# Kernel optimization log

Hardware: AMD Instinct MI355X
Metric: run time of the kernel (lower is better)

Reference implementation:

```python
import jax, jax.numpy as jnp
import numpy as np
import math

B, S, D, H = 2, 2048, 1024, 16
DK = D // H


def setup_inputs() -> dict:
    key = jax.random.key(0)
    ks = jax.random.split(key, 12)
    sc = 0.02
    inp = {
        "k": jax.random.normal(ks[0], (B, S, D), jnp.float32),
        "q": jax.random.normal(ks[1], (B, S, D), jnp.float32),
        "v": jax.random.normal(ks[2], (B, S, D), jnp.float32),
        "mask": 1,
        "w_k": jax.random.normal(ks[3], (D, D), jnp.float32) * sc,
        "b_k": jax.random.normal(ks[4], (D,), jnp.float32) * sc,
        "w_q": jax.random.normal(ks[5], (D, D), jnp.float32) * sc,
        "b_q": jax.random.normal(ks[6], (D,), jnp.float32) * sc,
        "w_v": jax.random.normal(ks[7], (D, D), jnp.float32) * sc,
        "b_v": jax.random.normal(ks[8], (D,), jnp.float32) * sc,
        "w_o": jax.random.normal(ks[9], (D, D), jnp.float32) * sc,
        "b_o": jax.random.normal(ks[10], (D,), jnp.float32) * sc,
    }
    return inp


def _mha(k, q, v, mask, w_k, b_k, w_q, b_q, w_v, b_v, w_o, b_o):
    # torch Linear: x @ W.T + b  (W is [out, in])
    key = k @ w_k.T + b_k
    query = q @ w_q.T + b_q
    value = v @ w_v.T + b_v
    # [B, S, D] -> [B, H, S, DK]
    key = key.reshape(B, S, H, DK).transpose(0, 2, 1, 3)
    query = query.reshape(B, S, H, DK).transpose(0, 2, 1, 3)
    value = value.reshape(B, S, H, DK).transpose(0, 2, 1, 3)
    # NOTE: original multiplies by sqrt(d_k) (not divides) -- faithful.
    scores = jnp.einsum("bhqd,bhkd->bhqk", query, key) * math.sqrt(DK)
    if mask:
        causal = jnp.triu(jnp.ones((S, S), dtype=bool), k=1)
        scores = jnp.where(causal, -jnp.inf, scores)
    # dropout p=0.0 is identity (original applies dropout to scores pre-softmax)
    attn = jax.nn.softmax(scores, axis=-1)
    out = jnp.einsum("bhqk,bhkd->bhqd", attn, value)
    out = out.transpose(0, 2, 1, 3).reshape(B, S, D)
    return out @ w_o.T + b_o


def reference(k, q, v, mask, w_k, b_k, w_q, b_q, w_v, b_v, w_o, b_o):
    return _mha(k, q, v, mask, w_k, b_k, w_q, b_q, w_v, b_v, w_o, b_o)
```

## Files before the change

kernel.cpp:

```cpp
#include <hip/hip_runtime.h>


typedef float f32x4 __attribute__((ext_vector_type(4)));
typedef float f32x16 __attribute__((ext_vector_type(16)));
typedef unsigned int u32x4 __attribute__((ext_vector_type(4)));
typedef _Float16 f16x8 __attribute__((ext_vector_type(8)));
typedef __fp16 fp16x2 __attribute__((ext_vector_type(2)));

#define DEV static __device__ __forceinline__

DEV unsigned short f2h(float x) {
  _Float16 h = (_Float16)x;
  union { _Float16 h; unsigned short u; } v; v.h = h;
  return v.u;
}

DEV unsigned pkrtz(float a, float b) {
  union { fp16x2 h; unsigned u; } v;
  v.h = __builtin_amdgcn_cvt_pkrtz(a, b);
  return v.u;
}

DEV float fexp2(float x) { return __builtin_amdgcn_exp2f(x); }

DEV void pswap(unsigned& a, unsigned& b) {
  auto r = __builtin_amdgcn_permlane32_swap(a, b, false, false);
  a = r[0]; b = r[1];
}

DEV void swap_pair(float v, float& x, float& y) {
  union { float f; unsigned u; } in; in.f = v;
  auto r = __builtin_amdgcn_permlane32_swap(in.u, in.u, false, false);
  union { unsigned u; float f; } ox, oy; ox.u = r[0]; oy.u = r[1];
  x = ox.f; y = oy.f;
}

DEV f16x8 mkfrag(unsigned a, unsigned b, unsigned c, unsigned d) {
  union { unsigned u[4]; f16x8 v; } z;
  z.u[0] = a; z.u[1] = b; z.u[2] = c; z.u[3] = d;
  return z.v;
}

DEV void mfma16(f32x4& d, u32x4 a, u32x4 b) {
  asm("v_mfma_f32_16x16x32_f16 %0, %1, %2, %0" : "+v"(d) : "v"(a), "v"(b));
}

DEV void gload16(const void* g, void* l) {
  __builtin_amdgcn_global_load_lds(
      (const __attribute__((address_space(1))) unsigned int*)g,
      (__attribute__((address_space(3))) unsigned int*)l, 16, 0, 0);
}

#define VMCNT0() asm volatile("s_waitcnt vmcnt(0)" ::: "memory")
#define NOPG(a,b,c,d)  asm volatile("s_nop 7\n\ts_nop 7" : "+v"(a), "+v"(b), "+v"(c), "+v"(d))

__global__ __launch_bounds__(256) void cvt_all(
    const float* __restrict__ k, const float* __restrict__ q, const float* __restrict__ v,
    const float* __restrict__ wk, const float* __restrict__ wq, const float* __restrict__ wv,
    const float* __restrict__ wo, unsigned short* __restrict__ dst) {
  const int i = (blockIdx.x * 256 + threadIdx.x) * 4;
  const float* src; int off;
  if (i < 4194304)       { src = k;  off = 0; }
  else if (i < 8388608)  { src = q;  off = 4194304; }
  else if (i < 12582912) { src = v;  off = 8388608; }
  else if (i < 13631488) { src = wk; off = 12582912; }
  else if (i < 14680064) { src = wq; off = 13631488; }
  else if (i < 15728640) { src = wv; off = 14680064; }
  else                   { src = wo; off = 15728640; }
  float4 val = *(const float4*)(src + (i - off));
  ushort4 o;
  o.x = f2h(val.x); o.y = f2h(val.y); o.z = f2h(val.z); o.w = f2h(val.w);
  *(ushort4*)(dst + i) = o;
}

DEV void gemm_body(const unsigned short* __restrict__ A, const unsigned short* __restrict__ W,
                   const float* __restrict__ bias, void* __restrict__ out, int mode,
                   float oscale) {
  __shared__ alignas(16) char lds_a[2][8192];
  __shared__ alignas(16) char lds_b[2][8192];
  const int t = threadIdx.x;
  const int l = t & 63, g = l >> 4, c = l & 15, w = t >> 6;
  const int wr = w >> 1, wc = w & 1;
  const int m0 = blockIdx.y << 7, n0 = blockIdx.x << 7;

  f32x4 acc[4][4] = {};

  const int i0 = t, i1 = t + 256;
  const int ar0 = i0 >> 2, as0 = (i0 & 3) ^ (ar0 & 3);
  const int ar1 = i1 >> 2, as1 = (i1 & 3) ^ (ar1 & 3);
  const unsigned short* ga0 = A + (long)(m0 + ar0) * 1024 + as0 * 8;
  const unsigned short* ga1 = A + (long)(m0 + ar1) * 1024 + as1 * 8;
  const unsigned short* gb0 = W + (long)(n0 + ar0) * 1024 + as0 * 8;
  const unsigned short* gb1 = W + (long)(n0 + ar1) * 1024 + as1 * 8;
  const int lo0 = i0 * 16, lo1 = i1 * 16;

  int aoff[4], boff[4];
#pragma unroll
  for (int i = 0; i < 4; i++) {
    const int ra = (wr << 6) + (i << 4) + c;
    aoff[i] = ra * 64 + ((g << 4) ^ ((ra & 3) << 4));
    const int rb = (wc << 6) + (i << 4) + c;
    boff[i] = rb * 64 + ((g << 4) ^ ((rb & 3) << 4));
  }

  gload16(ga0, lds_a[0] + lo0);
  gload16(ga1, lds_a[0] + lo1);
  gload16(gb0, lds_b[0] + lo0);
  gload16(gb1, lds_b[0] + lo1);

  for (int kt = 0; kt < 32; kt++) {
    const int cur = kt & 1;
    VMCNT0();
    __builtin_amdgcn_s_barrier();
    if (kt + 1 < 32) {
      gload16(ga0 + ((kt + 1) << 5), lds_a[cur ^ 1] + lo0);
      gload16(ga1 + ((kt + 1) << 5), lds_a[cur ^ 1] + lo1);
      gload16(gb0 + ((kt + 1) << 5), lds_b[cur ^ 1] + lo0);
      gload16(gb1 + ((kt + 1) << 5), lds_b[cur ^ 1] + lo1);
    }
    u32x4 af[4], bf[4];
#pragma unroll
    for (int i = 0; i < 4; i++) af[i] = *(const u32x4*)(lds_a[cur] + aoff[i]);
#pragma unroll
    for (int j = 0; j < 4; j++) bf[j] = *(const u32x4*)(lds_b[cur] + boff[j]);
#pragma unroll
    for (int i = 0; i < 4; i++)
#pragma unroll
      for (int j = 0; j < 4; j++)
        mfma16(acc[i][j], af[i], bf[j]);
  }

  NOPG(acc[0][0], acc[0][1], acc[0][2], acc[0][3]);
  NOPG(acc[1][0], acc[1][1], acc[1][2], acc[1][3]);
  NOPG(acc[2][0], acc[2][1], acc[2][2], acc[2][3]);
  NOPG(acc[3][0], acc[3][1], acc[3][2], acc[3][3]);

  if (mode == 1) {
#pragma unroll
    for (int j = 0; j < 4; j++) {
      const int n = n0 + (wc << 6) + (j << 4) + c;
      const float bb = bias[n];
      const int h = n >> 6, d = n & 63;
#pragma unroll
      for (int i = 0; i < 4; i++) {
        const int m = m0 + (wr << 6) + (i << 4) + (g << 2);
        const int b = m >> 11, s = m & 2047;
        ushort4 o;
        o.x = f2h(acc[i][j][0] + bb);
        o.y = f2h(acc[i][j][1] + bb);
        o.z = f2h(acc[i][j][2] + bb);
        o.w = f2h(acc[i][j][3] + bb);
        *(ushort4*)&((unsigned short*)out)[((long)((b << 4) + h) * 64 + d) * 2048 + s] = o;
      }
    }
  } else {
#pragma unroll
    for (int j = 0; j < 4; j++) {
      const int n = n0 + (wc << 6) + (j << 4) + c;
      const float bb = bias[n];
#pragma unroll
      for (int i = 0; i < 4; i++) {
#pragma unroll
        for (int r = 0; r < 4; r++) {
          const int m = m0 + (wr << 6) + (i << 4) + (g << 2) + r;
          const float val = (acc[i][j][r] + bb) * oscale;
          if (mode == 2) {
            ((float*)out)[(long)m * 1024 + n] = val;
          } else {
            const int b = m >> 11, s = m & 2047;
            const int h = n >> 6, d = n & 63;
            ((unsigned short*)out)[((long)((b << 4) + h) * 2048 + s) * 64 + d] = f2h(val);
          }
        }
      }
    }
  }
}

__global__ __launch_bounds__(256) void gemm_proj(
    const unsigned short* kb, const unsigned short* qb, const unsigned short* vb,
    const unsigned short* wkb, const unsigned short* wqb, const unsigned short* wvb,
    const float* bk, const float* bq, const float* bvv,
    unsigned short* Kp, unsigned short* Qp, unsigned short* VpT) {
  const int z = blockIdx.z;
  const unsigned short* A = (z == 0) ? kb : (z == 1) ? qb : vb;
  const unsigned short* W = (z == 0) ? wkb : (z == 1) ? wqb : wvb;
  const float* bias = (z == 0) ? bk : (z == 1) ? bq : bvv;
  void* out = (z == 0) ? (void*)Kp : (z == 1) ? (void*)Qp : (void*)VpT;
  const float sc = (z == 1) ? 11.5415603271f : 1.0f;
  gemm_body(A, W, bias, out, (z == 2) ? 1 : 0, sc);
}

__global__ __launch_bounds__(256) void gemm_out(
    const unsigned short* A, const unsigned short* W, const float* bias, float* out) {
  gemm_body(A, W, bias, out, 2, 1.0f);
}

__global__ __launch_bounds__(128) void attn_kernel(
    const unsigned short* __restrict__ Qp, const unsigned short* __restrict__ Kp,
    const unsigned short* __restrict__ VpT, unsigned short* __restrict__ O) {
  __shared__ alignas(16) char lds_k[2][8192];
  __shared__ alignas(16) char lds_v[2][8192];

  const int t = threadIdx.x;
  const int lane = t & 63, w = t >> 6;
  const int hi = lane >> 5, c32 = lane & 31;
  const int bh = blockIdx.x;
  const int qt = 31 - (int)blockIdx.y;
  const int qs = (qt << 6) + (w << 5);
  const int ntiles = qt + 1;

  const unsigned short* gk[4]; const unsigned short* gv[4]; int lofs[4];
#pragma unroll
  for (int n = 0; n < 4; n++) {
    const int idx = t + 128 * n;
    const int row = idx >> 3, sl = (idx & 7) ^ (row & 7);
    gk[n] = Kp + ((long)bh * 2048 + row) * 64 + sl * 8;
    gv[n] = VpT + ((long)bh * 64 + row) * 2048 + sl * 8;
    lofs[n] = idx * 16;
  }

  int koff[2][4];
#pragma unroll
  for (int x = 0; x < 2; x++)
#pragma unroll
    for (int y = 0; y < 4; y++) {
      const int row = 32 * x + c32;
      koff[x][y] = row * 128 + ((((y << 1) + hi) << 4) ^ ((row & 7) << 4));
    }

  const unsigned short* qrow = Qp + ((long)bh * 2048 + qs + c32) * 64 + hi * 8;
  f16x8 qf[4];
#pragma unroll
  for (int ks = 0; ks < 4; ks++) qf[ks] = *(const f16x8*)(qrow + ks * 16);

  f32x16 oT0 = {}, oT1 = {};
  float mrun = -1e30f, lrun = 0.f;
  const int qloc = (qs & 63) + c32;

#pragma unroll
  for (int n = 0; n < 4; n++) {
    gload16(gk[n], lds_k[0] + lofs[n]);
    gload16(gv[n], lds_v[0] + lofs[n]);
  }

  for (int tt = 0; tt < ntiles; tt++) {
    const int cur = tt & 1;
    VMCNT0();
    __builtin_amdgcn_s_barrier();
    if (tt + 1 < ntiles) {
      const long kvn = (long)(tt + 1) << 6;
#pragma unroll
      for (int n = 0; n < 4; n++) {
        gload16(gk[n] + kvn * 64, lds_k[cur ^ 1] + lofs[n]);
        gload16(gv[n] + kvn,      lds_v[cur ^ 1] + lofs[n]);
      }
    }

    f32x16 s0 = {}, s1 = {};
    __builtin_amdgcn_s_setprio(1);
#pragma unroll
    for (int ks = 0; ks < 4; ks++) {
      const f16x8 a0 = *(const f16x8*)(lds_k[cur] + koff[0][ks]);
      const f16x8 a1 = *(const f16x8*)(lds_k[cur] + koff[1][ks]);
      s0 = __builtin_amdgcn_mfma_f32_32x32x16_f16(a0, qf[ks], s0, 0, 0, 0);
      s1 = __builtin_amdgcn_mfma_f32_32x32x16_f16(a1, qf[ks], s1, 0, 0, 0);
    }
    __builtin_amdgcn_s_setprio(0);

    if (tt == qt) {
#pragma unroll
      for (int r = 0; r < 16; r++) {
        const int kvc = (r & 3) + 8 * (r >> 2) + 4 * hi;
        if (kvc > qloc)      s0[r] = -1e30f;
        if (kvc + 32 > qloc) s1[r] = -1e30f;
      }
    }

    float tm[16];
#pragma unroll
    for (int r = 0; r < 16; r++) tm[r] = fmaxf(s0[r], s1[r]);
#pragma unroll
    for (int d = 8; d >= 1; d >>= 1)
#pragma unroll
      for (int r = 0; r < 8; r++)
        if (r < d) tm[r] = fmaxf(tm[r], tm[r + d]);
    float x, y;
    swap_pair(tm[0], x, y);
    const float pmax = fmaxf(x, y);

    if (!__all(pmax - mrun <= 8.0f)) {
      const float mnew = fmaxf(mrun, pmax);
      const float corr = fexp2(mrun - mnew);
      mrun = mnew;
      lrun *= corr;
      oT0 *= corr;
      oT1 *= corr;
    }

#pragma unroll
    for (int r = 0; r < 16; r++) {
      s0[r] = fexp2(s0[r] - mrun);
      s1[r] = fexp2(s1[r] - mrun);
    }
    float ts[16];
#pragma unroll
    for (int r = 0; r < 16; r++) ts[r] = s0[r] + s1[r];
#pragma unroll
    for (int d = 8; d >= 1; d >>= 1)
#pragma unroll
      for (int r = 0; r < 8; r++)
        if (r < d) ts[r] = ts[r] + ts[r + d];
    lrun += ts[0];

    unsigned pk[8];
#pragma unroll
    for (int m = 0; m < 8; m++) pk[m] = pkrtz(s0[2 * m], s0[2 * m + 1]);
    pswap(pk[0], pk[2]); pswap(pk[1], pk[3]);
    pswap(pk[4], pk[6]); pswap(pk[5], pk[7]);
    const f16x8 pf0 = mkfrag(pk[0], pk[1], pk[2], pk[3]);
    const f16x8 pf1 = mkfrag(pk[4], pk[5], pk[6], pk[7]);
#pragma unroll
    for (int m = 0; m < 8; m++) pk[m] = pkrtz(s1[2 * m], s1[2 * m + 1]);
    pswap(pk[0], pk[2]); pswap(pk[1], pk[3]);
    pswap(pk[4], pk[6]); pswap(pk[5], pk[7]);
    const f16x8 pf2 = mkfrag(pk[0], pk[1], pk[2], pk[3]);
    const f16x8 pf3 = mkfrag(pk[4], pk[5], pk[6], pk[7]);

    __builtin_amdgcn_s_setprio(1);
    {
      const f16x8 v00 = *(const f16x8*)(lds_v[cur] + koff[0][0]);
      const f16x8 v01 = *(const f16x8*)(lds_v[cur] + koff[0][1]);
      const f16x8 v02 = *(const f16x8*)(lds_v[cur] + koff[0][2]);
      const f16x8 v03 = *(const f16x8*)(lds_v[cur] + koff[0][3]);
      oT0 = __builtin_amdgcn_mfma_f32_32x32x16_f16(v00, pf0, oT0, 0, 0, 0);
      oT0 = __builtin_amdgcn_mfma_f32_32x32x16_f16(v01, pf1, oT0, 0, 0, 0);
      oT0 = __builtin_amdgcn_mfma_f32_32x32x16_f16(v02, pf2, oT0, 0, 0, 0);
      oT0 = __builtin_amdgcn_mfma_f32_32x32x16_f16(v03, pf3, oT0, 0, 0, 0);
      const f16x8 v10 = *(const f16x8*)(lds_v[cur] + koff[1][0]);
      const f16x8 v11 = *(const f16x8*)(lds_v[cur] + koff[1][1]);
      const f16x8 v12 = *(const f16x8*)(lds_v[cur] + koff[1][2]);
      const f16x8 v13 = *(const f16x8*)(lds_v[cur] + koff[1][3]);
      oT1 = __builtin_amdgcn_mfma_f32_32x32x16_f16(v10, pf0, oT1, 0, 0, 0);
      oT1 = __builtin_amdgcn_mfma_f32_32x32x16_f16(v11, pf1, oT1, 0, 0, 0);
      oT1 = __builtin_amdgcn_mfma_f32_32x32x16_f16(v12, pf2, oT1, 0, 0, 0);
      oT1 = __builtin_amdgcn_mfma_f32_32x32x16_f16(v13, pf3, oT1, 0, 0, 0);
    }
    __builtin_amdgcn_s_setprio(0);
  }

  float sx, sy;
  swap_pair(lrun, sx, sy);
  const float inv = 1.0f / (sx + sy);
  const int b = bh >> 4, h = bh & 15;
  const long rowbase = ((long)b * 2048 + qs + c32) * 1024 + (h << 6);
#pragma unroll
  for (int dt = 0; dt < 2; dt++) {
#pragma unroll
    for (int g4 = 0; g4 < 4; g4++) {
      const f32x16& o = dt ? oT1 : oT0;
      uint2 pkd;
      pkd.x = pkrtz(o[4 * g4 + 0] * inv, o[4 * g4 + 1] * inv);
      pkd.y = pkrtz(o[4 * g4 + 2] * inv, o[4 * g4 + 3] * inv);
      *(uint2*)&O[rowbase + 32 * dt + 8 * g4 + 4 * hi] = pkd;
    }
  }
}

extern "C" void kernel_launch(void* const* d_in, const int* in_sizes, int n_in,
                              void* d_out, int out_size, void* d_ws, size_t ws_size,
                              hipStream_t stream) {
  (void)in_sizes; (void)n_in; (void)out_size; (void)ws_size;
  const float* kin = (const float*)d_in[0];
  const float* qin = (const float*)d_in[1];
  const float* vin = (const float*)d_in[2];
  const float* wk  = (const float*)d_in[4];
  const float* bk  = (const float*)d_in[5];
  const float* wq  = (const float*)d_in[6];
  const float* bq  = (const float*)d_in[7];
  const float* wv  = (const float*)d_in[8];
  const float* bv  = (const float*)d_in[9];
  const float* wo  = (const float*)d_in[10];
  const float* bo  = (const float*)d_in[11];

  unsigned short* ws  = (unsigned short*)d_ws;
  unsigned short* kb  = ws;
  unsigned short* qb  = ws + 4194304;
  unsigned short* vb  = ws + 8388608;
  unsigned short* wkb = ws + 12582912;
  unsigned short* wqb = ws + 13631488;
  unsigned short* wvb = ws + 14680064;
  unsigned short* wob = ws + 15728640;
  unsigned short* Kp  = ws + 16777216;
  unsigned short* Qp  = ws + 20971520;
  unsigned short* VpT = ws + 25165824;
  unsigned short* Oo  = ws + 29360128;

  cvt_all<<<16384, 256, 0, stream>>>(kin, qin, vin, wk, wq, wv, wo, ws);
  gemm_proj<<<dim3(8, 32, 3), 256, 0, stream>>>(kb, qb, vb, wkb, wqb, wvb,
                                                bk, bq, bv, Kp, Qp, VpT);
  attn_kernel<<<dim3(32, 32), 128, 0, stream>>>(Qp, Kp, VpT, Oo);
  gemm_out<<<dim3(8, 32), 256, 0, stream>>>(Oo, wob, bo, (float*)d_out);
}
```

Measured before the change: 130.5 us.

## Use single-wave attention blocks over 32-row query strips with 32-key tiles

The attention kernel changes from two-wave blocks covering 64 query rows with 64-key tiles to one-wave blocks covering 32 query rows with 32-key tiles. The grid doubles to 64 strips per head, and the V tile layout and swizzle are redone to fit the narrower tiles. The causal diagonal mask now covers only 32 keys, so less work is spent on masked-out entries, and the per-iteration block barrier is dropped. In exchange, K/V tiles are no longer shared between two waves, so global and LDS traffic per query row roughly doubles, and each iteration issues fewer MFMAs to amortize the softmax overhead.

```diff
diff --git a/kernel.cpp b/kernel.cpp
--- a/kernel.cpp
+++ b/kernel.cpp
@@ -1,11 +1,11 @@
 #include <hip/hip_runtime.h>
 
 
-typedef float f32x4 __attribute__((ext_vector_type(4)));
 typedef float f32x16 __attribute__((ext_vector_type(16)));
-typedef unsigned int u32x4 __attribute__((ext_vector_type(4)));
 typedef _Float16 f16x8 __attribute__((ext_vector_type(8)));
 typedef __fp16 fp16x2 __attribute__((ext_vector_type(2)));
+typedef float f32x4 __attribute__((ext_vector_type(4)));
+typedef unsigned int u32x4 __attribute__((ext_vector_type(4)));
 
 #define DEV static __device__ __forceinline__
 
@@ -196,37 +196,43 @@
   gemm_body(A, W, bias, out, 2, 1.0f);
 }
 
-__global__ __launch_bounds__(128) void attn_kernel(
+__global__ __launch_bounds__(64) void attn_kernel(
     const unsigned short* __restrict__ Qp, const unsigned short* __restrict__ Kp,
     const unsigned short* __restrict__ VpT, unsigned short* __restrict__ O) {
-  __shared__ alignas(16) char lds_k[2][8192];
-  __shared__ alignas(16) char lds_v[2][8192];
-
-  const int t = threadIdx.x;
-  const int lane = t & 63, w = t >> 6;
+  __shared__ alignas(16) char lds_k[2][4096];
+  __shared__ alignas(16) char lds_v[2][4096];
+
+  const int lane = threadIdx.x & 63;
   const int hi = lane >> 5, c32 = lane & 31;
   const int bh = blockIdx.x;
-  const int qt = 31 - (int)blockIdx.y;
-  const int qs = (qt << 6) + (w << 5);
-  const int ntiles = qt + 1;
-
-  const unsigned short* gk[4]; const unsigned short* gv[4]; int lofs[4];
+  const int strip = 63 - (int)blockIdx.y;
+  const int qs = strip << 5;
+  const int ntiles = strip + 1;
+
+  const unsigned short* gk[4]; const unsigned short* gv[4];
+  int lofsK[4], lofsV[4];
 #pragma unroll
   for (int n = 0; n < 4; n++) {
-    const int idx = t + 128 * n;
-    const int row = idx >> 3, sl = (idx & 7) ^ (row & 7);
-    gk[n] = Kp + ((long)bh * 2048 + row) * 64 + sl * 8;
-    gv[n] = VpT + ((long)bh * 64 + row) * 2048 + sl * 8;
-    lofs[n] = idx * 16;
-  }
-
-  int koff[2][4];
+    const int idx = lane + 64 * n;
+    const int rk = idx >> 3, sk = (idx & 7) ^ (rk & 7);
+    gk[n] = Kp + ((long)bh * 2048 + rk) * 64 + sk * 8;
+    lofsK[n] = idx * 16;
+    const int rv = idx >> 2, sv = (idx & 3) ^ ((rv >> 1) & 3);
+    gv[n] = VpT + ((long)bh * 64 + rv) * 2048 + sv * 8;
+    lofsV[n] = idx * 16;
+  }
+
+  int koffK[4];
+#pragma unroll
+  for (int ks = 0; ks < 4; ks++)
+    koffK[ks] = c32 * 128 + ((((ks << 1) + hi) ^ (c32 & 7)) << 4);
+  int koffV[2][2];
 #pragma unroll
   for (int x = 0; x < 2; x++)
 #pragma unroll
-    for (int y = 0; y < 4; y++) {
-      const int row = 32 * x + c32;
-      koff[x][y] = row * 128 + ((((y << 1) + hi) << 4) ^ ((row & 7) << 4));
+    for (int ks2 = 0; ks2 < 2; ks2++) {
+      const int row = (x << 5) + c32;
+      koffV[x][ks2] = row * 64 + (((((ks2 << 1) + hi)) ^ ((row >> 1) & 3)) << 4);
     }
 
   const unsigned short* qrow = Qp + ((long)bh * 2048 + qs + c32) * 64 + hi * 8;
@@ -236,54 +242,49 @@
 
   f32x16 oT0 = {}, oT1 = {};
   float mrun = -1e30f, lrun = 0.f;
-  const int qloc = (qs & 63) + c32;
 
 #pragma unroll
   for (int n = 0; n < 4; n++) {
-    gload16(gk[n], lds_k[0] + lofs[n]);
-    gload16(gv[n], lds_v[0] + lofs[n]);
+    gload16(gk[n], lds_k[0] + lofsK[n]);
+    gload16(gv[n], lds_v[0] + lofsV[n]);
   }
 
   for (int tt = 0; tt < ntiles; tt++) {
     const int cur = tt & 1;
     VMCNT0();
-    __builtin_amdgcn_s_barrier();
     if (tt + 1 < ntiles) {
-      const long kvn = (long)(tt + 1) << 6;
+      const long kvn = (long)(tt + 1) << 5;
 #pragma unroll
       for (int n = 0; n < 4; n++) {
-        gload16(gk[n] + kvn * 64, lds_k[cur ^ 1] + lofs[n]);
-        gload16(gv[n] + kvn,      lds_v[cur ^ 1] + lofs[n]);
+        gload16(gk[n] + kvn * 64, lds_k[cur ^ 1] + lofsK[n]);
+        gload16(gv[n] + kvn,      lds_v[cur ^ 1] + lofsV[n]);
       }
     }
 
-    f32x16 s0 = {}, s1 = {};
+    f32x16 s0 = {};
     __builtin_amdgcn_s_setprio(1);
 #pragma unroll
     for (int ks = 0; ks < 4; ks++) {
-      const f16x8 a0 = *(const f16x8*)(lds_k[cur] + koff[0][ks]);
-      const f16x8 a1 = *(const f16x8*)(lds_k[cur] + koff[1][ks]);
+      const f16x8 a0 = *(const f16x8*)(lds_k[cur] + koffK[ks]);
       s0 = __builtin_amdgcn_mfma_f32_32x32x16_f16(a0, qf[ks], s0, 0, 0, 0);
-      s1 = __builtin_amdgcn_mfma_f32_32x32x16_f16(a1, qf[ks], s1, 0, 0, 0);
     }
     __builtin_amdgcn_s_setprio(0);
 
-    if (tt == qt) {
+    if (tt == strip) {
 #pragma unroll
       for (int r = 0; r < 16; r++) {
         const int kvc = (r & 3) + 8 * (r >> 2) + 4 * hi;
-        if (kvc > qloc)      s0[r] = -1e30f;
-        if (kvc + 32 > qloc) s1[r] = -1e30f;
+        if (kvc > c32) s0[r] = -1e30f;
       }
     }
 
-    float tm[16];
-#pragma unroll
-    for (int r = 0; r < 16; r++) tm[r] = fmaxf(s0[r], s1[r]);
-#pragma unroll
-    for (int d = 8; d >= 1; d >>= 1)
-#pragma unroll
-      for (int r = 0; r < 8; r++)
+    float tm[8];
+#pragma unroll
+    for (int r = 0; r < 8; r++) tm[r] = fmaxf(s0[r], s0[r + 8]);
+#pragma unroll
+    for (int d = 4; d >= 1; d >>= 1)
+#pragma unroll
+      for (int r = 0; r < 4; r++)
         if (r < d) tm[r] = fmaxf(tm[r], tm[r + d]);
     float x, y;
     swap_pair(tm[0], x, y);
@@ -299,17 +300,14 @@
     }
 
 #pragma unroll
-    for (int r = 0; r < 16; r++) {
-      s0[r] = fexp2(s0[r] - mrun);
-      s1[r] = fexp2(s1[r] - mrun);
-    }
-    float ts[16];
-#pragma unroll
-    for (int r = 0; r < 16; r++) ts[r] = s0[r] + s1[r];
-#pragma unroll
-    for (int d = 8; d >= 1; d >>= 1)
-#pragma unroll
-      for (int r = 0; r < 8; r++)
+    for (int r = 0; r < 16; r++) s0[r] = fexp2(s0[r] - mrun);
+    float ts[8];
+#pragma unroll
+    for (int r = 0; r < 8; r++) ts[r] = s0[r] + s0[r + 8];
+#pragma unroll
+    for (int d = 4; d >= 1; d >>= 1)
+#pragma unroll
+      for (int r = 0; r < 4; r++)
         if (r < d) ts[r] = ts[r] + ts[r + d];
     lrun += ts[0];
 
@@ -320,31 +318,17 @@
     pswap(pk[4], pk[6]); pswap(pk[5], pk[7]);
     const f16x8 pf0 = mkfrag(pk[0], pk[1], pk[2], pk[3]);
     const f16x8 pf1 = mkfrag(pk[4], pk[5], pk[6], pk[7]);
-#pragma unroll
-    for (int m = 0; m < 8; m++) pk[m] = pkrtz(s1[2 * m], s1[2 * m + 1]);
-    pswap(pk[0], pk[2]); pswap(pk[1], pk[3]);
-    pswap(pk[4], pk[6]); pswap(pk[5], pk[7]);
-    const f16x8 pf2 = mkfrag(pk[0], pk[1], pk[2], pk[3]);
-    const f16x8 pf3 = mkfrag(pk[4], pk[5], pk[6], pk[7]);
 
     __builtin_amdgcn_s_setprio(1);
     {
-      const f16x8 v00 = *(const f16x8*)(lds_v[cur] + koff[0][0]);
-      const f16x8 v01 = *(const f16x8*)(lds_v[cur] + koff[0][1]);
-      const f16x8 v02 = *(const f16x8*)(lds_v[cur] + koff[0][2]);
-      const f16x8 v03 = *(const f16x8*)(lds_v[cur] + koff[0][3]);
+      const f16x8 v00 = *(const f16x8*)(lds_v[cur] + koffV[0][0]);
+      const f16x8 v01 = *(const f16x8*)(lds_v[cur] + koffV[0][1]);
       oT0 = __builtin_amdgcn_mfma_f32_32x32x16_f16(v00, pf0, oT0, 0, 0, 0);
       oT0 = __builtin_amdgcn_mfma_f32_32x32x16_f16(v01, pf1, oT0, 0, 0, 0);
-      oT0 = __builtin_amdgcn_mfma_f32_32x32x16_f16(v02, pf2, oT0, 0, 0, 0);
-      oT0 = __builtin_amdgcn_mfma_f32_32x32x16_f16(v03, pf3, oT0, 0, 0, 0);
-      const f16x8 v10 = *(const f16x8*)(lds_v[cur] + koff[1][0]);
-      const f16x8 v11 = *(const f16x8*)(lds_v[cur] + koff[1][1]);
-      const f16x8 v12 = *(const f16x8*)(lds_v[cur] + koff[1][2]);
-      const f16x8 v13 = *(const f16x8*)(lds_v[cur] + koff[1][3]);
+      const f16x8 v10 = *(const f16x8*)(lds_v[cur] + koffV[1][0]);
+      const f16x8 v11 = *(const f16x8*)(lds_v[cur] + koffV[1][1]);
       oT1 = __builtin_amdgcn_mfma_f32_32x32x16_f16(v10, pf0, oT1, 0, 0, 0);
       oT1 = __builtin_amdgcn_mfma_f32_32x32x16_f16(v11, pf1, oT1, 0, 0, 0);
-      oT1 = __builtin_amdgcn_mfma_f32_32x32x16_f16(v12, pf2, oT1, 0, 0, 0);
-      oT1 = __builtin_amdgcn_mfma_f32_32x32x16_f16(v13, pf3, oT1, 0, 0, 0);
     }
     __builtin_amdgcn_s_setprio(0);
   }
@@ -399,6 +383,6 @@
   cvt_all<<<16384, 256, 0, stream>>>(kin, qin, vin, wk, wq, wv, wo, ws);
   gemm_proj<<<dim3(8, 32, 3), 256, 0, stream>>>(kb, qb, vb, wkb, wqb, wvb,
                                                 bk, bq, bv, Kp, Qp, VpT);
-  attn_kernel<<<dim3(32, 32), 128, 0, stream>>>(Qp, Kp, VpT, Oo);
+  attn_kernel<<<dim3(32, 64), 64, 0, stream>>>(Qp, Kp, VpT, Oo);
   gemm_out<<<dim3(8, 32), 256, 0, stream>>>(Oo, wob, bo, (float*)d_out);
 }
```

Result: slower. 142.6 us (+9.3%).

## Fuse fp32-to-fp16 activation conversion into projection GEMM loads

Applied to the files above, without the earlier changes.

Removes the separate conversion pass over the k/q/v activations. The projection GEMM now reads fp32 rows directly into registers, converts them to fp16, and writes them to LDS, while the fp16 weights still stream through global_load_lds. The output GEMM becomes its own kernel. This avoids writing and re-reading about 24 MB of fp16 activations, but the projection loads now pass through registers with an extra LDS-write wait per k-step. The projection GEMM also reads fp32 activations, twice the bytes, up to 8 times across the N-tiles.

```diff
diff --git a/kernel.cpp b/kernel.cpp
--- a/kernel.cpp
+++ b/kernel.cpp
@@ -51,29 +51,34 @@
       (__attribute__((address_space(3))) unsigned int*)l, 16, 0, 0);
 }
 
+DEV u32x4 cvt8(float4 a, float4 b) {
+  union { unsigned short us[8]; u32x4 v; } z;
+  z.us[0] = f2h(a.x); z.us[1] = f2h(a.y); z.us[2] = f2h(a.z); z.us[3] = f2h(a.w);
+  z.us[4] = f2h(b.x); z.us[5] = f2h(b.y); z.us[6] = f2h(b.z); z.us[7] = f2h(b.w);
+  return z.v;
+}
+
 #define VMCNT0() asm volatile("s_waitcnt vmcnt(0)" ::: "memory")
+#define LGKMCNT0() asm volatile("s_waitcnt lgkmcnt(0)" ::: "memory")
 #define NOPG(a,b,c,d)  asm volatile("s_nop 7\n\ts_nop 7" : "+v"(a), "+v"(b), "+v"(c), "+v"(d))
 
-__global__ __launch_bounds__(256) void cvt_all(
-    const float* __restrict__ k, const float* __restrict__ q, const float* __restrict__ v,
-    const float* __restrict__ wk, const float* __restrict__ wq, const float* __restrict__ wv,
-    const float* __restrict__ wo, unsigned short* __restrict__ dst) {
+__global__ __launch_bounds__(256) void cvt_w(
+    const float* __restrict__ wk, const float* __restrict__ wq,
+    const float* __restrict__ wv, const float* __restrict__ wo,
+    unsigned short* __restrict__ dst) {
   const int i = (blockIdx.x * 256 + threadIdx.x) * 4;
   const float* src; int off;
-  if (i < 4194304)       { src = k;  off = 0; }
-  else if (i < 8388608)  { src = q;  off = 4194304; }
-  else if (i < 12582912) { src = v;  off = 8388608; }
-  else if (i < 13631488) { src = wk; off = 12582912; }
-  else if (i < 14680064) { src = wq; off = 13631488; }
-  else if (i < 15728640) { src = wv; off = 14680064; }
-  else                   { src = wo; off = 15728640; }
+  if (i < 1048576)      { src = wk; off = 0; }
+  else if (i < 2097152) { src = wq; off = 1048576; }
+  else if (i < 3145728) { src = wv; off = 2097152; }
+  else                  { src = wo; off = 3145728; }
   float4 val = *(const float4*)(src + (i - off));
   ushort4 o;
   o.x = f2h(val.x); o.y = f2h(val.y); o.z = f2h(val.z); o.w = f2h(val.w);
   *(ushort4*)(dst + i) = o;
 }
 
-DEV void gemm_body(const unsigned short* __restrict__ A, const unsigned short* __restrict__ W,
+DEV void proj_body(const float* __restrict__ A, const unsigned short* __restrict__ W,
                    const float* __restrict__ bias, void* __restrict__ out, int mode,
                    float oscale) {
   __shared__ alignas(16) char lds_a[2][8192];
@@ -88,8 +93,8 @@
   const int i0 = t, i1 = t + 256;
   const int ar0 = i0 >> 2, as0 = (i0 & 3) ^ (ar0 & 3);
   const int ar1 = i1 >> 2, as1 = (i1 & 3) ^ (ar1 & 3);
-  const unsigned short* ga0 = A + (long)(m0 + ar0) * 1024 + as0 * 8;
-  const unsigned short* ga1 = A + (long)(m0 + ar1) * 1024 + as1 * 8;
+  const float* gaf0 = A + (long)(m0 + ar0) * 1024 + as0 * 8;
+  const float* gaf1 = A + (long)(m0 + ar1) * 1024 + as1 * 8;
   const unsigned short* gb0 = W + (long)(n0 + ar0) * 1024 + as0 * 8;
   const unsigned short* gb1 = W + (long)(n0 + ar1) * 1024 + as1 * 8;
   const int lo0 = i0 * 16, lo1 = i1 * 16;
@@ -103,18 +108,28 @@
     boff[i] = rb * 64 + ((g << 4) ^ ((rb & 3) << 4));
   }
 
-  gload16(ga0, lds_a[0] + lo0);
-  gload16(ga1, lds_a[0] + lo1);
+  float4 r0a = *(const float4*)(gaf0);
+  float4 r0b = *(const float4*)(gaf0 + 4);
+  float4 r1a = *(const float4*)(gaf1);
+  float4 r1b = *(const float4*)(gaf1 + 4);
   gload16(gb0, lds_b[0] + lo0);
   gload16(gb1, lds_b[0] + lo1);
 
   for (int kt = 0; kt < 32; kt++) {
     const int cur = kt & 1;
     VMCNT0();
+    *(u32x4*)(lds_a[cur] + lo0) = cvt8(r0a, r0b);
+    *(u32x4*)(lds_a[cur] + lo1) = cvt8(r1a, r1b);
+    if (kt + 1 < 32) {
+      const int o = (kt + 1) << 5;
+      r0a = *(const float4*)(gaf0 + o);
+      r0b = *(const float4*)(gaf0 + o + 4);
+      r1a = *(const float4*)(gaf1 + o);
+      r1b = *(const float4*)(gaf1 + o + 4);
+    }
+    LGKMCNT0();
     __builtin_amdgcn_s_barrier();
     if (kt + 1 < 32) {
-      gload16(ga0 + ((kt + 1) << 5), lds_a[cur ^ 1] + lo0);
-      gload16(ga1 + ((kt + 1) << 5), lds_a[cur ^ 1] + lo1);
       gload16(gb0 + ((kt + 1) << 5), lds_b[cur ^ 1] + lo0);
       gload16(gb1 + ((kt + 1) << 5), lds_b[cur ^ 1] + lo1);
     }
@@ -164,13 +179,9 @@
         for (int r = 0; r < 4; r++) {
           const int m = m0 + (wr << 6) + (i << 4) + (g << 2) + r;
           const float val = (acc[i][j][r] + bb) * oscale;
-          if (mode == 2) {
-            ((float*)out)[(long)m * 1024 + n] = val;
-          } else {
-            const int b = m >> 11, s = m & 2047;
-            const int h = n >> 6, d = n & 63;
-            ((unsigned short*)out)[((long)((b << 4) + h) * 2048 + s) * 64 + d] = f2h(val);
-          }
+          const int b = m >> 11, s = m & 2047;
+          const int h = n >> 6, d = n & 63;
+          ((unsigned short*)out)[((long)((b << 4) + h) * 2048 + s) * 64 + d] = f2h(val);
         }
       }
     }
@@ -178,22 +189,94 @@
 }
 
 __global__ __launch_bounds__(256) void gemm_proj(
-    const unsigned short* kb, const unsigned short* qb, const unsigned short* vb,
+    const float* kf, const float* qf, const float* vf,
     const unsigned short* wkb, const unsigned short* wqb, const unsigned short* wvb,
     const float* bk, const float* bq, const float* bvv,
     unsigned short* Kp, unsigned short* Qp, unsigned short* VpT) {
   const int z = blockIdx.z;
-  const unsigned short* A = (z == 0) ? kb : (z == 1) ? qb : vb;
+  const float* A = (z == 0) ? kf : (z == 1) ? qf : vf;
   const unsigned short* W = (z == 0) ? wkb : (z == 1) ? wqb : wvb;
   const float* bias = (z == 0) ? bk : (z == 1) ? bq : bvv;
   void* out = (z == 0) ? (void*)Kp : (z == 1) ? (void*)Qp : (void*)VpT;
   const float sc = (z == 1) ? 11.5415603271f : 1.0f;
-  gemm_body(A, W, bias, out, (z == 2) ? 1 : 0, sc);
+  proj_body(A, W, bias, out, (z == 2) ? 1 : 0, sc);
 }
 
 __global__ __launch_bounds__(256) void gemm_out(
-    const unsigned short* A, const unsigned short* W, const float* bias, float* out) {
-  gemm_body(A, W, bias, out, 2, 1.0f);
+    const unsigned short* __restrict__ A, const unsigned short* __restrict__ W,
+    const float* __restrict__ bias, float* __restrict__ out) {
+  __shared__ alignas(16) char lds_a[2][8192];
+  __shared__ alignas(16) char lds_b[2][8192];
+  const int t = threadIdx.x;
+  const int l = t & 63, g = l >> 4, c = l & 15, w = t >> 6;
+  const int wr = w >> 1, wc = w & 1;
+  const int m0 = blockIdx.y << 7, n0 = blockIdx.x << 7;
+
+  f32x4 acc[4][4] = {};
+
+  const int i0 = t, i1 = t + 256;
+  const int ar0 = i0 >> 2, as0 = (i0 & 3) ^ (ar0 & 3);
+  const int ar1 = i1 >> 2, as1 = (i1 & 3) ^ (ar1 & 3);
+  const unsigned short* ga0 = A + (long)(m0 + ar0) * 1024 + as0 * 8;
+  const unsigned short* ga1 = A + (long)(m0 + ar1) * 1024 + as1 * 8;
+  const unsigned short* gb0 = W + (long)(n0 + ar0) * 1024 + as0 * 8;
+  const unsigned short* gb1 = W + (long)(n0 + ar1) * 1024 + as1 * 8;
+  const int lo0 = i0 * 16, lo1 = i1 * 16;
+
+  int aoff[4], boff[4];
+#pragma unroll
+  for (int i = 0; i < 4; i++) {
+    const int ra = (wr << 6) + (i << 4) + c;
+    aoff[i] = ra * 64 + ((g << 4) ^ ((ra & 3) << 4));
+    const int rb = (wc << 6) + (i << 4) + c;
+    boff[i] = rb * 64 + ((g << 4) ^ ((rb & 3) << 4));
+  }
+
+  gload16(ga0, lds_a[0] + lo0);
+  gload16(ga1, lds_a[0] + lo1);
+  gload16(gb0, lds_b[0] + lo0);
+  gload16(gb1, lds_b[0] + lo1);
+
+  for (int kt = 0; kt < 32; kt++) {
+    const int cur = kt & 1;
+    VMCNT0();
+    __builtin_amdgcn_s_barrier();
+    if (kt + 1 < 32) {
+      gload16(ga0 + ((kt + 1) << 5), lds_a[cur ^ 1] + lo0);
+      gload16(ga1 + ((kt + 1) << 5), lds_a[cur ^ 1] + lo1);
+      gload16(gb0 + ((kt + 1) << 5), lds_b[cur ^ 1] + lo0);
+      gload16(gb1 + ((kt + 1) << 5), lds_b[cur ^ 1] + lo1);
+    }
+    u32x4 af[4], bf[4];
+#pragma unroll
+    for (int i = 0; i < 4; i++) af[i] = *(const u32x4*)(lds_a[cur] + aoff[i]);
+#pragma unroll
+    for (int j = 0; j < 4; j++) bf[j] = *(const u32x4*)(lds_b[cur] + boff[j]);
+#pragma unroll
+    for (int i = 0; i < 4; i++)
+#pragma unroll
+      for (int j = 0; j < 4; j++)
+        mfma16(acc[i][j], af[i], bf[j]);
+  }
+
+  NOPG(acc[0][0], acc[0][1], acc[0][2], acc[0][3]);
+  NOPG(acc[1][0], acc[1][1], acc[1][2], acc[1][3]);
+  NOPG(acc[2][0], acc[2][1], acc[2][2], acc[2][3]);
+  NOPG(acc[3][0], acc[3][1], acc[3][2], acc[3][3]);
+
+#pragma unroll
+  for (int j = 0; j < 4; j++) {
+    const int n = n0 + (wc << 6) + (j << 4) + c;
+    const float bb = bias[n];
+#pragma unroll
+    for (int i = 0; i < 4; i++) {
+#pragma unroll
+      for (int r = 0; r < 4; r++) {
+        const int m = m0 + (wr << 6) + (i << 4) + (g << 2) + r;
+        out[(long)m * 1024 + n] = acc[i][j][r] + bb;
+      }
+    }
+  }
 }
 
 __global__ __launch_bounds__(128) void attn_kernel(
@@ -384,9 +467,6 @@
   const float* bo  = (const float*)d_in[11];
 
   unsigned short* ws  = (unsigned short*)d_ws;
-  unsigned short* kb  = ws;
-  unsigned short* qb  = ws + 4194304;
-  unsigned short* vb  = ws + 8388608;
   unsigned short* wkb = ws + 12582912;
   unsigned short* wqb = ws + 13631488;
   unsigned short* wvb = ws + 14680064;
@@ -396,8 +476,8 @@
   unsigned short* VpT = ws + 25165824;
   unsigned short* Oo  = ws + 29360128;
 
-  cvt_all<<<16384, 256, 0, stream>>>(kin, qin, vin, wk, wq, wv, wo, ws);
-  gemm_proj<<<dim3(8, 32, 3), 256, 0, stream>>>(kb, qb, vb, wkb, wqb, wvb,
+  cvt_w<<<4096, 256, 0, stream>>>(wk, wq, wv, wo, wkb);
+  gemm_proj<<<dim3(8, 32, 3), 256, 0, stream>>>(kin, qin, vin, wkb, wqb, wvb,
                                                 bk, bq, bv, Kp, Qp, VpT);
   attn_kernel<<<dim3(32, 32), 128, 0, stream>>>(Qp, Kp, VpT, Oo);
   gemm_out<<<dim3(8, 32), 256, 0, stream>>>(Oo, wob, bo, (float*)d_out);
```

Result: slower. 143.7 us (+10.1%).
